# Optimization experiments

Hardware: AMD Instinct MI355X
Metric: run time of the kernel (lower is better)

Reference implementation:

```python
import jax, jax.numpy as jnp
import numpy as np

B, Q, D = 8, 900, 256
NH, DH = 8, 32
FF = 1024
NLEVELS, NPOINTS, NLAYERS = 4, 4, 6
SHAPES = [(100, 100), (50, 50), (25, 25), (13, 13)]
S = sum(h * w for h, w in SHAPES)  # 13294
EPS = 1e-5
SCALE = 1.0 / float(np.sqrt(DH))


def layer_norm(x, g, b):
    mu = jnp.mean(x, -1, keepdims=True)
    var = jnp.var(x, -1, keepdims=True)
    return (x - mu) * jax.lax.rsqrt(var + EPS) * g + b


def mha(x, wi, bi, wo, bo):
    qkv = x @ wi.T + bi
    q, k, v = jnp.split(qkv, 3, axis=-1)
    q = q.reshape(B, Q, NH, DH)
    k = k.reshape(B, Q, NH, DH)
    v = v.reshape(B, Q, NH, DH)
    attn = jax.nn.softmax(jnp.einsum('bqhd,bkhd->bhqk', q, k) * SCALE, -1)
    o = jnp.einsum('bhqk,bkhd->bqhd', attn, v).reshape(B, Q, D)
    return o @ wo.T + bo


def msda_core(value, loc, aw):
    # value (B,S,NH,DH); loc (B,Q,NH,L,P,2) in [0,1]; aw (B,Q,NH,L,P)
    v = value.transpose(0, 2, 1, 3)  # (B,NH,S,DH)
    out = jnp.zeros((B, NH, Q, DH), value.dtype)
    start = 0
    for lvl, (H_, W_) in enumerate(SHAPES):
        vl = v[:, :, start:start + H_ * W_]  # (B,NH,HW,DH)
        start += H_ * W_
        l = loc[:, :, :, lvl].transpose(0, 2, 1, 3, 4).reshape(B, NH, Q * NPOINTS, 2)
        # grid_sample align_corners=False pixel coords
        x = l[..., 0] * W_ - 0.5
        y = l[..., 1] * H_ - 0.5
        x0 = jnp.floor(x)
        y0 = jnp.floor(y)
        wx = x - x0
        wy = y - y0
        g = jnp.zeros((B, NH, Q * NPOINTS, DH), value.dtype)
        for dy, dx, w in ((0, 0, (1 - wx) * (1 - wy)), (0, 1, wx * (1 - wy)),
                          (1, 0, (1 - wx) * wy), (1, 1, wx * wy)):
            xi = x0 + dx
            yi = y0 + dy
            valid = ((xi >= 0) & (xi < W_) & (yi >= 0) & (yi < H_)).astype(value.dtype)
            idx = (jnp.clip(yi, 0, H_ - 1) * W_ + jnp.clip(xi, 0, W_ - 1)).astype(jnp.int32)
            gi = jnp.take_along_axis(vl, idx[..., None], axis=2)  # (B,NH,QP,DH)
            g = g + gi * (w * valid)[..., None]
        g = g.reshape(B, NH, Q, NPOINTS, DH)
        a = aw[:, :, :, lvl].transpose(0, 2, 1, 3)  # (B,NH,Q,P)
        out = out + jnp.einsum('bhqpd,bhqp->bhqd', g, a)
    return out.transpose(0, 2, 1, 3).reshape(B, Q, D)


def msda(query, ref, value_in, vp_w, vp_b, so_w, so_b, aw_w, aw_b, op_w, op_b):
    value = (value_in @ vp_w.T + vp_b).reshape(B, S, NH, DH)
    off = (query @ so_w.T + so_b).reshape(B, Q, NH, NLEVELS, NPOINTS, 2)
    aw = (query @ aw_w.T + aw_b).reshape(B, Q, NH, NLEVELS * NPOINTS)
    aw = jax.nn.softmax(aw, -1).reshape(B, Q, NH, NLEVELS, NPOINTS)
    # offset normalizer is (W, H) per level
    norm = jnp.array([[w, h] for h, w in SHAPES], jnp.float32)
    loc = ref[:, :, None, :, None, :] + off / norm[None, None, None, :, None, :]
    return msda_core(value, loc, aw) @ op_w.T + op_b


def setup_inputs():
    key = jax.random.key(0)
    it = iter(jax.random.split(key, 32))

    def rn(shape, s=0.02):
        return jax.random.normal(next(it), shape, jnp.float32) * s

    z = lambda n: jnp.zeros((n,), jnp.float32)
    o = lambda n: jnp.ones((n,), jnp.float32)
    NOFF = NH * NLEVELS * NPOINTS
    return {
        'tgt': rn((B, Q, D), 1.0),
        'reference_points': jax.random.uniform(next(it), (B, Q, 2), jnp.float32),
        'memory': rn((B, S, D), 1.0),
        'spatial_shapes': jnp.array(SHAPES, jnp.int32),
        'level_start_index': jnp.array(np.cumsum([0] + [h * w for h, w in SHAPES[:-1]]), jnp.int32),
        'valid_ratios': jnp.ones((B, NLEVELS, 2), jnp.float32),
        'query_pos': rn((B, Q, D), 1.0),
        'sa_in_w': rn((3 * D, D)), 'sa_in_b': z(3 * D),
        'sa_out_w': rn((D, D)), 'sa_out_b': z(D),
        'n1_g': o(D), 'n1_b': z(D),
        'n2_g': o(D), 'n2_b': z(D),
        'n3_g': o(D), 'n3_b': z(D),
        'vp_w': rn((D, D)), 'vp_b': z(D),
        'so_w': rn((NOFF * 2, D)), 'so_b': rn((NOFF * 2,), 0.5),
        'aw_w': rn((NOFF, D)), 'aw_b': z(NOFF),
        'op_w': rn((D, D)), 'op_b': z(D),
        'ff1_w': rn((FF, D)), 'ff1_b': z(FF),
        'ff2_w': rn((D, FF)), 'ff2_b': z(D),
    }


def reference(tgt, reference_points, memory, spatial_shapes, level_start_index,
              valid_ratios, query_pos,
              sa_in_w, sa_in_b, sa_out_w, sa_out_b,
              n1_g, n1_b, n2_g, n2_b, n3_g, n3_b,
              vp_w, vp_b, so_w, so_b, aw_w, aw_b, op_w, op_b,
              ff1_w, ff1_b, ff2_w, ff2_b):
    # NOTE: nn.ModuleList([decoder_layer]*num_layers) in the source shares one
    # layer's weights across all 6 layers; bbox_embed is None so reference
    # points are constant across layers.
    output = tgt
    ref_input = reference_points[:, :, None, :] * valid_ratios[:, None, :, :]  # (B,Q,L,2)
    inter, inter_refs = [], []
    for _ in range(NLAYERS):
        output = output + query_pos
        t2 = mha(output, sa_in_w, sa_in_b, sa_out_w, sa_out_b)
        output = layer_norm(output + t2, n1_g, n1_b)
        t2 = msda(output, ref_input, memory, vp_w, vp_b, so_w, so_b, aw_w, aw_b, op_w, op_b)
        output = layer_norm(output + t2, n2_g, n2_b)
        t2 = jax.nn.relu(output @ ff1_w.T + ff1_b) @ ff2_w.T + ff2_b
        output = layer_norm(output + t2, n3_g, n3_b)
        inter.append(output)
        inter_refs.append(reference_points)
    return (jnp.stack(inter), jnp.stack(inter_refs))
```

## Files before the change

### kernel.cpp

```cpp
#include <hip/hip_runtime.h>
#include <hip/hip_bf16.h>

typedef __hip_bfloat16 bf16;
typedef __bf16 bf16x8 __attribute__((ext_vector_type(8)));
typedef float  f32x4  __attribute__((ext_vector_type(4)));

#define NB 8
#define NQ 900
#define DM 256
#define NHEADS 8
#define DHEAD 32
#define NFF 1024
#define NLAY 6
#define NS 13294
#define BQ (NB*NQ)
#define LN_EPS 1e-5f
#define ATT_SCALE 0.17677669529663687f
#define SAK 40
#define VWS 264
#define PSK 88

__device__ __forceinline__ float bfd(const bf16* p, size_t i){ return __bfloat162float(p[i]); }

__device__ __forceinline__ float ldv(const void* p, size_t i, int mode, bool extF32)
{
    if (mode == 0) return ((const float*)p)[i];
    if (mode == 1) return bfd((const bf16*)p, i);
    return extF32 ? ((const float*)p)[i] : bfd((const bf16*)p, i);
}

__device__ __forceinline__ void unpack8(uint4 u, float* t)
{
    t[0] = __uint_as_float((u.x & 0xffffu) << 16);
    t[1] = __uint_as_float(u.x & 0xffff0000u);
    t[2] = __uint_as_float((u.y & 0xffffu) << 16);
    t[3] = __uint_as_float(u.y & 0xffff0000u);
    t[4] = __uint_as_float((u.z & 0xffffu) << 16);
    t[5] = __uint_as_float(u.z & 0xffff0000u);
    t[6] = __uint_as_float((u.w & 0xffffu) << 16);
    t[7] = __uint_as_float(u.w & 0xffff0000u);
}

__global__ __launch_bounds__(256) void detect_dtype(const void* __restrict__ tgt,
        float* __restrict__ flag)
{
    __shared__ float red[256];
    int t = threadIdx.x;
    const unsigned short* u = (const unsigned short*)tgt;
    float m = 0.f;
    for (int i = t; i < 2048; i += 256) {
        unsigned int bits = ((unsigned int)u[i]) << 16;
        float v = fabsf(__uint_as_float(bits));
        if (!isfinite(v)) v = 1e30f;
        m = fmaxf(m, v);
    }
    red[t] = m;
    __syncthreads();
    for (int st = 128; st; st >>= 1) {
        if (t < st) red[t] = fmaxf(red[t], red[t + st]);
        __syncthreads();
    }
    if (t == 0) flag[0] = (red[0] > 1e8f) ? 1.f : 0.f;
}

__global__ __launch_bounds__(256) void convert_w(const void* __restrict__ src,
        bf16* __restrict__ dst, const float* __restrict__ flagp)
{
    const bool ef = flagp[0] > 0.5f;
    size_t base = ((size_t)blockIdx.x * 256 + threadIdx.x) * 8;
    if (ef) {
        const float* s = (const float*)src + base;
        float4 f0 = *(const float4*)s;
        float4 f1 = *(const float4*)(s + 4);
        union { bf16 a[8]; uint4 u; } t;
        t.a[0] = __float2bfloat16(f0.x); t.a[1] = __float2bfloat16(f0.y);
        t.a[2] = __float2bfloat16(f0.z); t.a[3] = __float2bfloat16(f0.w);
        t.a[4] = __float2bfloat16(f1.x); t.a[5] = __float2bfloat16(f1.y);
        t.a[6] = __float2bfloat16(f1.z); t.a[7] = __float2bfloat16(f1.w);
        *(uint4*)(dst + base) = t.u;
    } else {
        *(uint4*)(dst + base) = *(const uint4*)((const bf16*)src + base);
    }
}

__global__ __launch_bounds__(256, 2) void gemm_vp(const void* __restrict__ A,
        const bf16* __restrict__ Wb, const void* __restrict__ bias,
        bf16* __restrict__ C, int M, const float* __restrict__ flagp)
{
    const bool ef = flagp[0] > 0.5f;
    __shared__ __align__(16) bf16 Al[64 * VWS];
    const int tid = threadIdx.x;
    const int w = tid >> 6, lane = tid & 63, lm = lane & 15, lq = lane >> 4;
    const int wq = w * 64;

    bf16x8 wf[4][8];
    #pragma unroll
    for (int nt = 0; nt < 4; nt++)
        #pragma unroll
        for (int ks = 0; ks < 8; ks++)
            wf[nt][ks] = *(const bf16x8*)(Wb +
                (size_t)(wq + nt * 16 + lm) * 256 + ks * 32 + lq * 8);

    float bv[4];
    #pragma unroll
    for (int nt = 0; nt < 4; nt++) bv[nt] = ldv(bias, wq + nt * 16 + lm, 2, ef);

    const int arow_l = tid >> 2;
    const int asub   = tid & 3;

    const int ntiles = (M + 63) / 64;
    for (int tile = blockIdx.x; tile < ntiles; tile += gridDim.x) {
        const int m0 = tile * 64;
        __syncthreads();
        {
            const int grow = m0 + arow_l;
            if (grow < M) {
                if (ef) {
                    const float* ap = (const float*)A + (size_t)grow * 256;
                    #pragma unroll
                    for (int j = 0; j < 16; j++) {
                        int colf = j * 16 + asub * 4;
                        float4 f = *(const float4*)(ap + colf);
                        union { bf16 a[4]; uint2 u; } t;
                        t.a[0] = __float2bfloat16(f.x); t.a[1] = __float2bfloat16(f.y);
                        t.a[2] = __float2bfloat16(f.z); t.a[3] = __float2bfloat16(f.w);
                        *(uint2*)&Al[arow_l * VWS + colf] = t.u;
                    }
                } else {
                    const bf16* ap = (const bf16*)A + (size_t)grow * 256;
                    #pragma unroll
                    for (int j = 0; j < 8; j++) {
                        int cole = j * 32 + asub * 8;
                        *(uint4*)&Al[arow_l * VWS + cole] = *(const uint4*)(ap + cole);
                    }
                }
            } else {
                uint4 z = make_uint4(0u, 0u, 0u, 0u);
                #pragma unroll
                for (int j = 0; j < 8; j++)
                    *(uint4*)&Al[arow_l * VWS + j * 32 + asub * 8] = z;
            }
        }
        __syncthreads();

        f32x4 acc[4][4];
        #pragma unroll
        for (int mi = 0; mi < 4; mi++)
            #pragma unroll
            for (int nt = 0; nt < 4; nt++)
                acc[mi][nt] = (f32x4){0.f, 0.f, 0.f, 0.f};

        #pragma unroll
        for (int ks = 0; ks < 8; ks++) {
            bf16x8 af[4];
            #pragma unroll
            for (int mi = 0; mi < 4; mi++)
                af[mi] = *(const bf16x8*)&Al[(mi * 16 + lm) * VWS + ks * 32 + lq * 8];
            #pragma unroll
            for (int nt = 0; nt < 4; nt++)
                #pragma unroll
                for (int mi = 0; mi < 4; mi++)
                    acc[mi][nt] = __builtin_amdgcn_mfma_f32_16x16x32_bf16(
                                      af[mi], wf[nt][ks], acc[mi][nt], 0, 0, 0);
        }

        #pragma unroll
        for (int mi = 0; mi < 4; mi++) {
            #pragma unroll
            for (int r = 0; r < 4; r++) {
                int m = m0 + mi * 16 + lq * 4 + r;
                if (m >= M) continue;
                #pragma unroll
                for (int nt = 0; nt < 4; nt++) {
                    int col = wq + nt * 16 + lm;
                    C[(size_t)m * 256 + col] = __float2bfloat16(acc[mi][nt][r] + bv[nt]);
                }
            }
        }
    }
}

__global__ __launch_bounds__(256, 2) void gemm_wreg(const bf16* __restrict__ A,
        const bf16* __restrict__ Wb, const void* __restrict__ bias,
        void* __restrict__ C, int cmode, int M, int N, int relu,
        const float* __restrict__ flagp)
{
    const bool ef = flagp[0] > 0.5f;
    __shared__ __align__(16) bf16 Al[32 * VWS];
    const int tid = threadIdx.x;
    const int w = tid >> 6, lane = tid & 63, lm = lane & 15, lq = lane >> 4;
    const int n0 = blockIdx.x * 256;
    const int m0 = blockIdx.y * 32;
    const int wq = n0 + w * 64;

    bf16x8 wf[4][8];
    #pragma unroll
    for (int nt = 0; nt < 4; nt++)
        #pragma unroll
        for (int ks = 0; ks < 8; ks++)
            wf[nt][ks] = *(const bf16x8*)(Wb +
                (size_t)(wq + nt * 16 + lm) * 256 + ks * 32 + lq * 8);

    float bv[4];
    #pragma unroll
    for (int nt = 0; nt < 4; nt++) bv[nt] = ldv(bias, wq + nt * 16 + lm, 2, ef);

    {
        const int ar = tid >> 3, ac = (tid & 7) * 32;
        if (m0 + ar < M) {
            const bf16* ap = A + (size_t)(m0 + ar) * 256 + ac;
            #pragma unroll
            for (int j = 0; j < 4; j++)
                *(uint4*)&Al[ar * VWS + ac + j * 8] = *(const uint4*)(ap + j * 8);
        } else {
            uint4 z = make_uint4(0u, 0u, 0u, 0u);
            #pragma unroll
            for (int j = 0; j < 4; j++)
                *(uint4*)&Al[ar * VWS + ac + j * 8] = z;
        }
    }
    __syncthreads();

    f32x4 acc[2][4];
    #pragma unroll
    for (int mi = 0; mi < 2; mi++)
        #pragma unroll
        for (int nt = 0; nt < 4; nt++)
            acc[mi][nt] = (f32x4){0.f, 0.f, 0.f, 0.f};

    #pragma unroll
    for (int ks = 0; ks < 8; ks++) {
        bf16x8 af[2];
        #pragma unroll
        for (int mi = 0; mi < 2; mi++)
            af[mi] = *(const bf16x8*)&Al[(mi * 16 + lm) * VWS + ks * 32 + lq * 8];
        #pragma unroll
        for (int nt = 0; nt < 4; nt++)
            #pragma unroll
            for (int mi = 0; mi < 2; mi++)
                acc[mi][nt] = __builtin_amdgcn_mfma_f32_16x16x32_bf16(
                                  af[mi], wf[nt][ks], acc[mi][nt], 0, 0, 0);
    }

    #pragma unroll
    for (int mi = 0; mi < 2; mi++) {
        #pragma unroll
        for (int r = 0; r < 4; r++) {
            int m = m0 + mi * 16 + lq * 4 + r;
            if (m >= M) continue;
            #pragma unroll
            for (int nt = 0; nt < 4; nt++) {
                int col = wq + nt * 16 + lm;
                float v = acc[mi][nt][r] + bv[nt];
                if (relu) v = fmaxf(v, 0.f);
                size_t ci = (size_t)m * N + col;
                if (cmode == 0) ((float*)C)[ci] = v;
                else            ((bf16*)C)[ci] = __float2bfloat16(v);
            }
        }
    }
}

__global__ __launch_bounds__(256, 2) void gemm_lnw(const bf16* __restrict__ A,
        const bf16* __restrict__ Wb, const void* __restrict__ bias,
        const float* __restrict__ res, const void* __restrict__ gw,
        const void* __restrict__ bw, float* __restrict__ out32,
        bf16* __restrict__ outbf, void* __restrict__ dout, size_t obase,
        const void* __restrict__ qp, int M,
        const float* __restrict__ flagp)
{
    const bool ef = flagp[0] > 0.5f;
    __shared__ __align__(16) bf16 Al[32 * VWS];
    const int tid = threadIdx.x;
    const int w = tid >> 6, lane = tid & 63, lm = lane & 15, lq = lane >> 4;
    const int m0 = blockIdx.y * 32;
    const int wq = w * 64;

    bf16x8 wf[4][8];
    #pragma unroll
    for (int nt = 0; nt < 4; nt++)
        #pragma unroll
        for (int ks = 0; ks < 8; ks++)
            wf[nt][ks] = *(const bf16x8*)(Wb +
                (size_t)(wq + nt * 16 + lm) * 256 + ks * 32 + lq * 8);

    float bias_c[4];
    #pragma unroll
    for (int nt = 0; nt < 4; nt++) bias_c[nt] = ldv(bias, wq + nt * 16 + lm, 2, ef);

    {
        const int ar = tid >> 3, ac = (tid & 7) * 32;
        if (m0 + ar < M) {
            const bf16* ap = A + (size_t)(m0 + ar) * 256 + ac;
            #pragma unroll
            for (int j = 0; j < 4; j++)
                *(uint4*)&Al[ar * VWS + ac + j * 8] = *(const uint4*)(ap + j * 8);
        } else {
            uint4 z = make_uint4(0u, 0u, 0u, 0u);
            #pragma unroll
            for (int j = 0; j < 4; j++)
                *(uint4*)&Al[ar * VWS + ac + j * 8] = z;
        }
    }
    __syncthreads();

    f32x4 acc[2][4];
    #pragma unroll
    for (int mi = 0; mi < 2; mi++)
        #pragma unroll
        for (int nt = 0; nt < 4; nt++)
            acc[mi][nt] = (f32x4){0.f, 0.f, 0.f, 0.f};

    #pragma unroll
    for (int ks = 0; ks < 8; ks++) {
        bf16x8 af[2];
        #pragma unroll
        for (int mi = 0; mi < 2; mi++)
            af[mi] = *(const bf16x8*)&Al[(mi * 16 + lm) * VWS + ks * 32 + lq * 8];
        #pragma unroll
        for (int nt = 0; nt < 4; nt++)
            #pragma unroll
            for (int mi = 0; mi < 2; mi++)
                acc[mi][nt] = __builtin_amdgcn_mfma_f32_16x16x32_bf16(
                                  af[mi], wf[nt][ks], acc[mi][nt], 0, 0, 0);
    }

    #pragma unroll
    for (int mi = 0; mi < 2; mi++)
        #pragma unroll
        for (int r = 0; r < 4; r++) {
            int row = m0 + mi * 16 + lq * 4 + r;
            bool vr_ = row < M;
            #pragma unroll
            for (int nt = 0; nt < 4; nt++) {
                int col = wq + nt * 16 + lm;
                float rv = vr_ ? res[(size_t)row * DM + col] : 0.f;
                acc[mi][nt][r] += bias_c[nt] + rv;
            }
        }

    __syncthreads();
    float* red = (float*)Al;
    float mu[2][4], rstd[2][4];
    #pragma unroll
    for (int mi = 0; mi < 2; mi++)
        #pragma unroll
        for (int r = 0; r < 4; r++) {
            float s = acc[mi][0][r] + acc[mi][1][r] + acc[mi][2][r] + acc[mi][3][r];
            s += __shfl_xor(s, 1, 64); s += __shfl_xor(s, 2, 64);
            s += __shfl_xor(s, 4, 64); s += __shfl_xor(s, 8, 64);
            if (lm == 0) red[(mi * 16 + lq * 4 + r) * 4 + w] = s;
        }
    __syncthreads();
    #pragma unroll
    for (int mi = 0; mi < 2; mi++)
        #pragma unroll
        for (int r = 0; r < 4; r++) {
            int ri = mi * 16 + lq * 4 + r;
            mu[mi][r] = (red[ri*4] + red[ri*4+1] + red[ri*4+2] + red[ri*4+3]) * (1.f / DM);
        }
    #pragma unroll
    for (int mi = 0; mi < 2; mi++)
        #pragma unroll
        for (int r = 0; r < 4; r++) {
            float q = 0.f;
            #pragma unroll
            for (int nt = 0; nt < 4; nt++) {
                float d = acc[mi][nt][r] - mu[mi][r];
                q += d * d;
            }
            q += __shfl_xor(q, 1, 64); q += __shfl_xor(q, 2, 64);
            q += __shfl_xor(q, 4, 64); q += __shfl_xor(q, 8, 64);
            if (lm == 0) red[128 + (mi * 16 + lq * 4 + r) * 4 + w] = q;
        }
    __syncthreads();
    #pragma unroll
    for (int mi = 0; mi < 2; mi++)
        #pragma unroll
        for (int r = 0; r < 4; r++) {
            int ri = mi * 16 + lq * 4 + r;
            float var = (red[128+ri*4] + red[128+ri*4+1] + red[128+ri*4+2] + red[128+ri*4+3]) * (1.f / DM);
            rstd[mi][r] = rsqrtf(var + LN_EPS);
        }

    float gcol[4], bcol[4];
    #pragma unroll
    for (int nt = 0; nt < 4; nt++) {
        int col = wq + nt * 16 + lm;
        gcol[nt] = ldv(gw, col, 2, ef);
        bcol[nt] = ldv(bw, col, 2, ef);
    }
    #pragma unroll
    for (int mi = 0; mi < 2; mi++)
        #pragma unroll
        for (int r = 0; r < 4; r++) {
            int row = m0 + mi * 16 + lq * 4 + r;
            if (row >= M) continue;
            size_t rbase = (size_t)row * DM;
            #pragma unroll
            for (int nt = 0; nt < 4; nt++) {
                int col = wq + nt * 16 + lm;
                float o = (acc[mi][nt][r] - mu[mi][r]) * rstd[mi][r] * gcol[nt] + bcol[nt];
                if (dout) {
                    if (ef) ((float*)dout)[obase + rbase + col] = o;
                    else    ((bf16*)dout)[obase + rbase + col] = __float2bfloat16(o);
                }
                float o2 = o + (qp ? ldv(qp, rbase + col, 2, ef) : 0.f);
                out32[rbase + col] = o2;
                outbf[rbase + col] = __float2bfloat16(o2);
            }
        }
}

__device__ __forceinline__ void stage_a32(bf16* As, const void* A, bool a_bf16,
        int m0, int M, int K, int k0, int tid)
{
    const int row = tid >> 3, col = (tid & 7) * 4;
    const int arow = m0 + row;
    union { bf16 a[4]; uint2 u; } t;
    if (arow < M) {
        size_t base = (size_t)arow * K + k0 + col;
        if (a_bf16) {
            t.u = *(const uint2*)((const bf16*)A + base);
        } else {
            float4 f = *(const float4*)((const float*)A + base);
            t.a[0] = __float2bfloat16(f.x); t.a[1] = __float2bfloat16(f.y);
            t.a[2] = __float2bfloat16(f.z); t.a[3] = __float2bfloat16(f.w);
        }
    } else {
        t.u = make_uint2(0u, 0u);
    }
    *(uint2*)&As[row * SAK + col] = t.u;
}

__global__ __launch_bounds__(256) void gemm_ln(const bf16* __restrict__ A,
        const bf16* __restrict__ Wb, const void* __restrict__ bias,
        const float* __restrict__ res, const void* __restrict__ gw,
        const void* __restrict__ bw, float* __restrict__ out32,
        bf16* __restrict__ outbf, void* __restrict__ dout, size_t obase,
        const void* __restrict__ qp, int M, int K,
        const float* __restrict__ flagp)
{
    const bool ef = flagp[0] > 0.5f;
    __shared__ __align__(16) bf16 As[32 * SAK];
    __shared__ __align__(16) bf16 Ws[256 * SAK];
    const int tid = threadIdx.x;
    const int m0 = blockIdx.y * 32;
    const int w = tid >> 6, lane = tid & 63, lm = lane & 15, lq = lane >> 4;
    const int wr = w >> 1, wc = w & 1;
    const int srow = tid >> 2, scol = (tid & 3) * 8;

    f32x4 acc[8];
    #pragma unroll
    for (int nt = 0; nt < 8; nt++) acc[nt] = (f32x4){0.f, 0.f, 0.f, 0.f};

    for (int k0 = 0; k0 < K; k0 += 32) {
        stage_a32(As, A, true, m0, M, K, k0, tid);
        #pragma unroll
        for (int it = 0; it < 4; it++) {
            int rr = it * 64 + srow;
            *(uint4*)&Ws[rr * SAK + scol] =
                *(const uint4*)(Wb + (size_t)rr * K + k0 + scol);
        }
        __syncthreads();

        bf16x8 af = *(const bf16x8*)&As[(wr * 16 + lm) * SAK + lq * 8];
        #pragma unroll
        for (int nt = 0; nt < 8; nt++) {
            bf16x8 bfr = *(const bf16x8*)&Ws[(wc * 128 + nt * 16 + lm) * SAK + lq * 8];
            acc[nt] = __builtin_amdgcn_mfma_f32_16x16x32_bf16(af, bfr, acc[nt], 0, 0, 0);
        }
        __syncthreads();
    }

    float bias_c[8], gcol[8], bcol[8];
    #pragma unroll
    for (int nt = 0; nt < 8; nt++) {
        int col = wc * 128 + nt * 16 + lm;
        bias_c[nt] = ldv(bias, col, 2, ef);
        gcol[nt]   = ldv(gw,   col, 2, ef);
        bcol[nt]   = ldv(bw,   col, 2, ef);
    }
    #pragma unroll
    for (int r = 0; r < 4; r++) {
        int row = m0 + wr * 16 + lq * 4 + r;
        bool vr_ = row < M;
        #pragma unroll
        for (int nt = 0; nt < 8; nt++) {
            int col = wc * 128 + nt * 16 + lm;
            float rv = vr_ ? res[(size_t)row * DM + col] : 0.f;
            acc[nt][r] += bias_c[nt] + rv;
        }
    }

    float* red = (float*)As;
    float mu[4], rstd[4];
    #pragma unroll
    for (int r = 0; r < 4; r++) {
        float s = 0.f;
        #pragma unroll
        for (int nt = 0; nt < 8; nt++) s += acc[nt][r];
        s += __shfl_xor(s, 1, 64); s += __shfl_xor(s, 2, 64);
        s += __shfl_xor(s, 4, 64); s += __shfl_xor(s, 8, 64);
        if (lm == 0) red[(wr * 16 + lq * 4 + r) * 2 + wc] = s;
    }
    __syncthreads();
    #pragma unroll
    for (int r = 0; r < 4; r++) {
        int rl = wr * 16 + lq * 4 + r;
        mu[r] = (red[rl * 2] + red[rl * 2 + 1]) * (1.f / DM);
    }
    #pragma unroll
    for (int r = 0; r < 4; r++) {
        float q = 0.f;
        #pragma unroll
        for (int nt = 0; nt < 8; nt++) {
            float d = acc[nt][r] - mu[r];
            q += d * d;
        }
        q += __shfl_xor(q, 1, 64); q += __shfl_xor(q, 2, 64);
        q += __shfl_xor(q, 4, 64); q += __shfl_xor(q, 8, 64);
        if (lm == 0) red[64 + (wr * 16 + lq * 4 + r) * 2 + wc] = q;
    }
    __syncthreads();
    #pragma unroll
    for (int r = 0; r < 4; r++) {
        int rl = wr * 16 + lq * 4 + r;
        float var = (red[64 + rl * 2] + red[64 + rl * 2 + 1]) * (1.f / DM);
        rstd[r] = rsqrtf(var + LN_EPS);
    }

    #pragma unroll
    for (int r = 0; r < 4; r++) {
        int row = m0 + wr * 16 + lq * 4 + r;
        if (row >= M) continue;
        size_t rbase = (size_t)row * DM;
        #pragma unroll
        for (int nt = 0; nt < 8; nt++) {
            int col = wc * 128 + nt * 16 + lm;
            float o = (acc[nt][r] - mu[r]) * rstd[r] * gcol[nt] + bcol[nt];
            if (dout) {
                if (ef) ((float*)dout)[obase + rbase + col] = o;
                else    ((bf16*)dout)[obase + rbase + col] = __float2bfloat16(o);
            }
            float o2 = o + (qp ? ldv(qp, rbase + col, 2, ef) : 0.f);
            out32[rbase + col] = o2;
            outbf[rbase + col] = __float2bfloat16(o2);
        }
    }
}

__global__ __launch_bounds__(256) void gemm_soaw(const bf16* __restrict__ A,
        const bf16* __restrict__ Wb, const void* __restrict__ b1,
        const void* __restrict__ b2, float* __restrict__ C1,
        float* __restrict__ C2, int M, const float* __restrict__ flagp)
{
    const bool ef = flagp[0] > 0.5f;
    const int K = DM;
    __shared__ __align__(16) bf16 As[32 * SAK];
    __shared__ __align__(16) bf16 Ws[128 * SAK];
    const int tid = threadIdx.x;
    const int m0 = blockIdx.y * 32, n0 = blockIdx.x * 128;
    const int w = tid >> 6, lane = tid & 63, lm = lane & 15, lq = lane >> 4;
    const int wr = w >> 1, wc = w & 1;
    const int srow = tid >> 2, scol = (tid & 3) * 8;

    f32x4 acc[4];
    #pragma unroll
    for (int nt = 0; nt < 4; nt++) acc[nt] = (f32x4){0.f, 0.f, 0.f, 0.f};

    for (int k0 = 0; k0 < K; k0 += 32) {
        stage_a32(As, A, true, m0, M, K, k0, tid);
        #pragma unroll
        for (int it = 0; it < 2; it++) {
            int rr = it * 64 + srow;
            *(uint4*)&Ws[rr * SAK + scol] =
                *(const uint4*)(Wb + (size_t)(n0 + rr) * K + k0 + scol);
        }
        __syncthreads();

        bf16x8 af = *(const bf16x8*)&As[(wr * 16 + lm) * SAK + lq * 8];
        #pragma unroll
        for (int nt = 0; nt < 4; nt++) {
            bf16x8 bfr = *(const bf16x8*)&Ws[(wc * 64 + nt * 16 + lm) * SAK + lq * 8];
            acc[nt] = __builtin_amdgcn_mfma_f32_16x16x32_bf16(af, bfr, acc[nt], 0, 0, 0);
        }
        __syncthreads();
    }

    float* Cd; const void* bsrc; int nst, c0;
    if (n0 < 256) { Cd = C1; bsrc = b1; nst = 256; c0 = n0; }
    else          { Cd = C2; bsrc = b2; nst = 128; c0 = n0 - 256; }

    #pragma unroll
    for (int nt = 0; nt < 4; nt++) {
        int cl = wc * 64 + nt * 16 + lm;
        float bv = ldv(bsrc, c0 + cl, 2, ef);
        #pragma unroll
        for (int r = 0; r < 4; r++) {
            int m = m0 + wr * 16 + lq * 4 + r;
            if (m >= M) continue;
            Cd[(size_t)m * nst + c0 + cl] = acc[nt][r] + bv;
        }
    }
}

__global__ __launch_bounds__(256) void add_qpos(const void* __restrict__ a, int amode,
        const void* __restrict__ qp, float* __restrict__ o, bf16* __restrict__ ob,
        const float* __restrict__ flagp)
{
    const bool ef = flagp[0] > 0.5f;
    int i = blockIdx.x * 256 + threadIdx.x;
    float v = ldv(a, i, amode, ef) + ldv(qp, i, 2, ef);
    o[i]  = v;
    ob[i] = __float2bfloat16(v);
}

__global__ __launch_bounds__(256) void mha_mfma(const bf16* __restrict__ qkv,
        bf16* __restrict__ out)
{
    const int qt = blockIdx.x, h = blockIdx.y, b = blockIdx.z;
    const int q0 = qt * 64;
    const int tid = threadIdx.x;
    const int w = tid >> 6, lane = tid & 63;
    const int lm = lane & 15, lq = lane >> 4;
    const int srow = tid >> 2, sc = (tid & 3) * 8;

    __shared__ __align__(16) bf16 Qs[64][SAK];
    __shared__ __align__(16) bf16 Ks[64][SAK];
    __shared__ __align__(16) bf16 Vt[32][66];
    __shared__ __align__(16) bf16 Ps[64][PSK];

    const bf16* base = qkv + (size_t)b * NQ * 768;

    {
        bf16 tmp[8];
        if (q0 + srow < NQ) {
            uint4 u = *(const uint4*)(base + (size_t)(q0 + srow) * 768 + h * DHEAD + sc);
            float t[8]; unpack8(u, t);
            #pragma unroll
            for (int i = 0; i < 8; i++) tmp[i] = __float2bfloat16(t[i] * ATT_SCALE);
        } else {
            #pragma unroll
            for (int i = 0; i < 8; i++) tmp[i] = __float2bfloat16(0.f);
        }
        *(uint4*)&Qs[srow][sc] = *(const uint4*)tmp;
    }
    __syncthreads();
    const bf16x8 qf = *(const bf16x8*)&Qs[w * 16 + lm][lq * 8];

    f32x4 O[2] = {{0.f,0.f,0.f,0.f},{0.f,0.f,0.f,0.f}};
    float mrow = -1e30f, lrow = 0.f;

    for (int k0 = 0; k0 < NQ; k0 += 64) {
        __syncthreads();
        {
            uint4 uk = {0u,0u,0u,0u}, uv = {0u,0u,0u,0u};
            if (k0 + srow < NQ) {
                const bf16* rp = base + (size_t)(k0 + srow) * 768 + h * DHEAD + sc;
                uk = *(const uint4*)(rp + 256);
                uv = *(const uint4*)(rp + 512);
            }
            *(uint4*)&Ks[srow][sc] = uk;
            const bf16* vv = (const bf16*)&uv;
            #pragma unroll
            for (int i = 0; i < 8; i++) Vt[sc + i][srow] = vv[i];
        }
        __syncthreads();

        float sv[16];
        #pragma unroll
        for (int mt = 0; mt < 4; mt++) {
            bf16x8 kf = *(const bf16x8*)&Ks[mt * 16 + lm][lq * 8];
            f32x4 d = __builtin_amdgcn_mfma_f32_16x16x32_bf16(kf, qf,
                        (f32x4){0.f,0.f,0.f,0.f}, 0, 0, 0);
            sv[mt*4+0] = d[0]; sv[mt*4+1] = d[1]; sv[mt*4+2] = d[2]; sv[mt*4+3] = d[3];
        }
        #pragma unroll
        for (int mt = 0; mt < 4; mt++)
            #pragma unroll
            for (int r = 0; r < 4; r++)
                if (k0 + mt * 16 + lq * 4 + r >= NQ) sv[mt*4+r] = -1e30f;

        float tmax = sv[0];
        #pragma unroll
        for (int j = 1; j < 16; j++) tmax = fmaxf(tmax, sv[j]);
        tmax = fmaxf(tmax, __shfl_xor(tmax, 16, 64));
        tmax = fmaxf(tmax, __shfl_xor(tmax, 32, 64));
        float mnew = fmaxf(mrow, tmax);
        float alpha = __expf(mrow - mnew);
        mrow = mnew;
        float psum = 0.f;
        #pragma unroll
        for (int j = 0; j < 16; j++) {
            float p = __expf(sv[j] - mnew);
            sv[j] = p; psum += p;
        }
        psum += __shfl_xor(psum, 16, 64);
        psum += __shfl_xor(psum, 32, 64);
        lrow = lrow * alpha + psum;

        #pragma unroll
        for (int mt = 0; mt < 4; mt++) {
            union { bf16 a[4]; uint2 u; } pw;
            #pragma unroll
            for (int r = 0; r < 4; r++) pw.a[r] = __float2bfloat16(sv[mt*4+r]);
            *(uint2*)&Ps[w * 16 + lm][mt * 16 + lq * 4] = pw.u;
        }

        #pragma unroll
        for (int mt = 0; mt < 2; mt++)
            #pragma unroll
            for (int r = 0; r < 4; r++) O[mt][r] *= alpha;
        #pragma unroll
        for (int ks = 0; ks < 2; ks++) {
            bf16x8 pf = *(const bf16x8*)&Ps[w * 16 + lm][ks * 32 + lq * 8];
            #pragma unroll
            for (int mt = 0; mt < 2; mt++) {
                bf16x8 vf = *(const bf16x8*)&Vt[mt * 16 + lm][ks * 32 + lq * 8];
                O[mt] = __builtin_amdgcn_mfma_f32_16x16x32_bf16(vf, pf, O[mt], 0, 0, 0);
            }
        }
    }

    int q = q0 + w * 16 + lm;
    if (q < NQ) {
        float invl = 1.f / lrow;
        bf16* op = out + ((size_t)(b * NQ + q)) * DM + h * DHEAD;
        #pragma unroll
        for (int mt = 0; mt < 2; mt++)
            #pragma unroll
            for (int r = 0; r < 4; r++)
                op[mt * 16 + lq * 4 + r] = __float2bfloat16(O[mt][r] * invl);
    }
}

__global__ __launch_bounds__(256) void msda_sample8(const bf16* __restrict__ value,
        const float* __restrict__ off, const float* __restrict__ aw,
        const void* __restrict__ refp, const void* __restrict__ vr,
        bf16* __restrict__ out, const float* __restrict__ flagp)
{
    const bool ef = flagp[0] > 0.5f;
    const int tid = threadIdx.x;
    const int bq0 = blockIdx.x * 8;

    __shared__ float sOff[8][256];
    __shared__ float sAw[8][128];
    __shared__ float sref[8][2];
    __shared__ float svrq[8][8];

    {
        const float* osrc = off + (size_t)bq0 * 256;
        #pragma unroll
        for (int i = 0; i < 2; i++) {
            int e = i * 1024 + tid * 4;
            *(float4*)&sOff[e >> 8][e & 255] = *(const float4*)(osrc + e);
        }
        int e2 = tid * 4;
        *(float4*)&sAw[e2 >> 7][e2 & 127] = *(const float4*)(aw + (size_t)bq0 * 128 + e2);
    }
    if (tid < 16) sref[tid >> 1][tid & 1] = ldv(refp, (size_t)(bq0 + (tid >> 1)) * 2 + (tid & 1), 2, ef);
    if (tid < 64) {
        int qi = tid >> 3, j = tid & 7;
        int b = (bq0 + qi) / NQ;
        svrq[qi][j] = ldv(vr, b * 8 + j, 2, ef);
    }
    __syncthreads();

    if (tid < 64) {
        int qi = tid >> 3, h = tid & 7;
        float* p = &sAw[qi][h * 16];
        float mx = -1e30f;
        #pragma unroll
        for (int j = 0; j < 16; j++) mx = fmaxf(mx, p[j]);
        float s = 0.f;
        #pragma unroll
        for (int j = 0; j < 16; j++) { float e = __expf(p[j] - mx); p[j] = e; s += e; }
        float inv = 1.f / s;
        #pragma unroll
        for (int j = 0; j < 16; j++) p[j] *= inv;
    }
    __syncthreads();

    const int qi = tid >> 5, sub = tid & 31;
    const int h = sub >> 2, cg = sub & 3;
    const int bq = bq0 + qi;
    const int b = bq / NQ;
    const bf16* vb = value + (size_t)b * NS * DM + h * DHEAD + cg * 8;

    float acc[8];
    #pragma unroll
    for (int j = 0; j < 8; j++) acc[j] = 0.f;

    const int HS[4] = {100, 50, 25, 13};
    const int ST[4] = {0, 10000, 12500, 13125};
    #pragma unroll
    for (int lvl = 0; lvl < 4; lvl++) {
        const int W_ = HS[lvl], H_ = HS[lvl], st = ST[lvl];
        float rx = sref[qi][0] * svrq[qi][lvl * 2 + 0] * (float)W_;
        float ry = sref[qi][1] * svrq[qi][lvl * 2 + 1] * (float)H_;
        #pragma unroll
        for (int p = 0; p < 4; p++) {
            int oi = h * 32 + lvl * 8 + p * 2;
            float x = fminf(fmaxf(rx + sOff[qi][oi]     - 0.5f, -4.f), (float)W_ + 4.f);
            float y = fminf(fmaxf(ry + sOff[qi][oi + 1] - 0.5f, -4.f), (float)H_ + 4.f);
            float x0f = floorf(x), y0f = floorf(y);
            float wx = x - x0f, wy = y - y0f;
            int x0 = (int)x0f, y0 = (int)y0f;
            int x1i = x0 + 1, y1i = y0 + 1;
            bool vx0 = (x0 >= 0) && (x0 < W_), vx1 = (x1i >= 0) && (x1i < W_);
            bool vy0 = (y0 >= 0) && (y0 < H_), vy1 = (y1i >= 0) && (y1i < H_);
            float g[8];
            #pragma unroll
            for (int j = 0; j < 8; j++) g[j] = 0.f;
            float t[8];
            if (vy0) {
                int rowo = (st + y0 * W_) * DM;
                if (vx0) {
                    uint4 u = *(const uint4*)(vb + rowo + x0 * DM);
                    unpack8(u, t);
                    float wgt = (1.f - wx) * (1.f - wy);
                    #pragma unroll
                    for (int j = 0; j < 8; j++) g[j] += wgt * t[j];
                }
                if (vx1) {
                    uint4 u = *(const uint4*)(vb + rowo + x1i * DM);
                    unpack8(u, t);
                    float wgt = wx * (1.f - wy);
                    #pragma unroll
                    for (int j = 0; j < 8; j++) g[j] += wgt * t[j];
                }
            }
            if (vy1) {
                int rowo = (st + y1i * W_) * DM;
                if (vx0) {
                    uint4 u = *(const uint4*)(vb + rowo + x0 * DM);
                    unpack8(u, t);
                    float wgt = (1.f - wx) * wy;
                    #pragma unroll
                    for (int j = 0; j < 8; j++) g[j] += wgt * t[j];
                }
                if (vx1) {
                    uint4 u = *(const uint4*)(vb + rowo + x1i * DM);
                    unpack8(u, t);
                    float wgt = wx * wy;
                    #pragma unroll
                    for (int j = 0; j < 8; j++) g[j] += wgt * t[j];
                }
            }
            float a = sAw[qi][h * 16 + lvl * 4 + p];
            #pragma unroll
            for (int j = 0; j < 8; j++) acc[j] += a * g[j];
        }
    }

    union { bf16 t[8]; uint4 u; } pk;
    #pragma unroll
    for (int j = 0; j < 8; j++) pk.t[j] = __float2bfloat16(acc[j]);
    *(uint4*)(out + (size_t)bq * DM + h * DHEAD + cg * 8) = pk.u;
}

__global__ __launch_bounds__(256) void copy_refs(const void* __restrict__ refp,
        void* __restrict__ out, const float* __restrict__ flagp)
{
    const bool ef = flagp[0] > 0.5f;
    int i = blockIdx.x * 256 + threadIdx.x;
    if (i >= NLAY * BQ * 2) return;
    float v = ldv(refp, i % (BQ * 2), 2, ef);
    size_t oi = (size_t)NLAY * BQ * DM + i;
    if (ef) ((float*)out)[oi] = v;
    else    ((bf16*)out)[oi] = __float2bfloat16(v);
}

extern "C" void kernel_launch(void* const* d_in, const int* in_sizes, int n_in,
                              void* d_out, int out_size, void* d_ws, size_t ws_size,
                              hipStream_t stream)
{
    const void* tgt     = d_in[0];
    const void* refp    = d_in[1];
    const void* memory  = d_in[2];
    const void* vr      = d_in[5];
    const void* qp      = d_in[6];
    const void* sa_in_w = d_in[7];
    const void* sa_in_b = d_in[8];
    const void* sa_out_w= d_in[9];
    const void* sa_out_b= d_in[10];
    const void* n1_g    = d_in[11];
    const void* n1_b    = d_in[12];
    const void* n2_g    = d_in[13];
    const void* n2_b    = d_in[14];
    const void* n3_g    = d_in[15];
    const void* n3_b    = d_in[16];
    const void* vp_w    = d_in[17];
    const void* vp_b    = d_in[18];
    const void* so_w    = d_in[19];
    const void* so_b    = d_in[20];
    const void* aw_w    = d_in[21];
    const void* aw_b    = d_in[22];
    const void* op_w    = d_in[23];
    const void* op_b    = d_in[24];
    const void* ff1_w   = d_in[25];
    const void* ff1_b   = d_in[26];
    const void* ff2_w   = d_in[27];
    const void* ff2_b   = d_in[28];

    char* w = (char*)d_ws;
    float* flagp  = (float*)w;  w += 256;
    bf16*  value  = (bf16*)w;   w += (size_t)NB * NS * DM * 2;
    float* outbuf = (float*)w;  w += (size_t)BQ * DM * 4;
    float* x1samp = (float*)w;  w += (size_t)BQ * DM * 4;
    bf16*  bigb   = (bf16*)w;   w += (size_t)BQ * NFF * 2;
    float* attoff = (float*)w;  w += (size_t)BQ * DM * 4;
    float* awb    = (float*)w;  w += (size_t)BQ * 128 * 4;
    bf16*  abuf   = (bf16*)w;   w += (size_t)BQ * DM * 2;
    bf16*  outbf  = (bf16*)w;   w += (size_t)BQ * DM * 2;
    bf16* wb_sa_in = (bf16*)w;  w += (size_t)768 * 256 * 2;
    bf16* wb_sa_out= (bf16*)w;  w += (size_t)256 * 256 * 2;
    bf16* wb_soaw  = (bf16*)w;  w += (size_t)384 * 256 * 2;
    bf16* wb_op    = (bf16*)w;  w += (size_t)256 * 256 * 2;
    bf16* wb_ff1   = (bf16*)w;  w += (size_t)NFF * 256 * 2;
    bf16* wb_ff2   = (bf16*)w;  w += (size_t)256 * NFF * 2;
    bf16* wb_vp    = (bf16*)w;  w += (size_t)256 * 256 * 2;

    const int gy = (BQ + 31) / 32;
    const int MV = NB * NS;

    detect_dtype<<<1, 256, 0, stream>>>(tgt, flagp);
    convert_w<<< 96, 256, 0, stream>>>(sa_in_w,  wb_sa_in,  flagp);
    convert_w<<< 32, 256, 0, stream>>>(sa_out_w, wb_sa_out, flagp);
    convert_w<<< 32, 256, 0, stream>>>(so_w,     wb_soaw,   flagp);
    convert_w<<< 16, 256, 0, stream>>>(aw_w,     wb_soaw + 256 * 256, flagp);
    convert_w<<< 32, 256, 0, stream>>>(op_w,     wb_op,     flagp);
    convert_w<<<128, 256, 0, stream>>>(ff1_w,    wb_ff1,    flagp);
    convert_w<<<128, 256, 0, stream>>>(ff2_w,    wb_ff2,    flagp);
    convert_w<<< 32, 256, 0, stream>>>(vp_w,     wb_vp,     flagp);

    gemm_vp<<<512, 256, 0, stream>>>(memory, wb_vp, vp_b, value, MV, flagp);

    copy_refs<<<(NLAY * BQ * 2 + 255) / 256, 256, 0, stream>>>(refp, d_out, flagp);

    add_qpos<<<BQ * DM / 256, 256, 0, stream>>>(tgt, 2, qp, x1samp, abuf, flagp);

    for (int l = 0; l < NLAY; l++) {
        gemm_wreg<<<dim3(3, gy), 256, 0, stream>>>(
            abuf, wb_sa_in, sa_in_b, bigb, 1, BQ, 768, 0, flagp);
        mha_mfma<<<dim3(15, NHEADS, NB), 256, 0, stream>>>(bigb, abuf);
        gemm_lnw<<<dim3(1, gy), 256, 0, stream>>>(
            abuf, wb_sa_out, sa_out_b, x1samp, n1_g, n1_b,
            outbuf, outbf, nullptr, 0, nullptr, BQ, flagp);

        gemm_soaw<<<dim3(3, gy), 256, 0, stream>>>(
            outbf, wb_soaw, so_b, aw_b, attoff, awb, BQ, flagp);
        msda_sample8<<<BQ / 8, 256, 0, stream>>>(value, attoff, awb, refp, vr, abuf, flagp);
        gemm_lnw<<<dim3(1, gy), 256, 0, stream>>>(
            abuf, wb_op, op_b, outbuf, n2_g, n2_b,
            outbuf, outbf, nullptr, 0, nullptr, BQ, flagp);

        gemm_wreg<<<dim3(4, gy), 256, 0, stream>>>(
            outbf, wb_ff1, ff1_b, bigb, 1, BQ, 1024, 1, flagp);
        gemm_ln<<<dim3(1, gy), 256, 0, stream>>>(
            bigb, wb_ff2, ff2_b, outbuf, n3_g, n3_b,
            x1samp, abuf, d_out, (size_t)l * BQ * DM, qp, BQ, NFF, flagp);
    }
}
```

Baseline: 1.486 ms.

## Halve row tile of LN-fused GEMMs and restage FF2 with resident A rows

The fused GEMM+LayerNorm kernel for the attention and deformable-attention output projections now processes 16 rows per block instead of 32. This doubles the grid (450 vs 225 blocks) so more CUs are busy, and it uses a small dedicated reduction buffer. The FF2+LN kernel is replaced by gemm_ffln, which keeps a full 16x1024 A tile in shared memory and streams the 256-wide weight in 64-K chunks, with each wave owning 64 output columns. The trade-off is that each block re-reads the whole weight matrix for half as many rows, doubling total weight traffic, and the kernel uses a large LDS footprint (~69KB), which may limit occupancy.

Result: slower. 1.523 ms (+2.5%).

```diff
diff --git a/kernel.cpp b/kernel.cpp
--- a/kernel.cpp
+++ b/kernel.cpp
@@ -19,6 +19,8 @@
 #define SAK 40
 #define VWS 264
 #define PSK 88
+#define AFS 1032
+#define WS2 72
 
 __device__ __forceinline__ float bfd(const bf16* p, size_t i){ return __bfloat162float(p[i]); }
 
@@ -270,10 +272,11 @@
         const float* __restrict__ flagp)
 {
     const bool ef = flagp[0] > 0.5f;
-    __shared__ __align__(16) bf16 Al[32 * VWS];
+    __shared__ __align__(16) bf16 Al[16 * VWS];
+    __shared__ float red[128];
     const int tid = threadIdx.x;
     const int w = tid >> 6, lane = tid & 63, lm = lane & 15, lq = lane >> 4;
-    const int m0 = blockIdx.y * 32;
+    const int m0 = blockIdx.y * 16;
     const int wq = w * 64;
 
     bf16x8 wf[4][8];
@@ -289,99 +292,77 @@
     for (int nt = 0; nt < 4; nt++) bias_c[nt] = ldv(bias, wq + nt * 16 + lm, 2, ef);
 
     {
-        const int ar = tid >> 3, ac = (tid & 7) * 32;
+        const int ar = tid >> 4, ac = (tid & 15) * 16;
         if (m0 + ar < M) {
             const bf16* ap = A + (size_t)(m0 + ar) * 256 + ac;
-            #pragma unroll
-            for (int j = 0; j < 4; j++)
-                *(uint4*)&Al[ar * VWS + ac + j * 8] = *(const uint4*)(ap + j * 8);
+            *(uint4*)&Al[ar * VWS + ac]     = *(const uint4*)ap;
+            *(uint4*)&Al[ar * VWS + ac + 8] = *(const uint4*)(ap + 8);
         } else {
             uint4 z = make_uint4(0u, 0u, 0u, 0u);
-            #pragma unroll
-            for (int j = 0; j < 4; j++)
-                *(uint4*)&Al[ar * VWS + ac + j * 8] = z;
-        }
-    }
-    __syncthreads();
-
-    f32x4 acc[2][4];
-    #pragma unroll
-    for (int mi = 0; mi < 2; mi++)
+            *(uint4*)&Al[ar * VWS + ac]     = z;
+            *(uint4*)&Al[ar * VWS + ac + 8] = z;
+        }
+    }
+    __syncthreads();
+
+    f32x4 acc[4];
+    #pragma unroll
+    for (int nt = 0; nt < 4; nt++) acc[nt] = (f32x4){0.f, 0.f, 0.f, 0.f};
+
+    #pragma unroll
+    for (int ks = 0; ks < 8; ks++) {
+        bf16x8 af = *(const bf16x8*)&Al[lm * VWS + ks * 32 + lq * 8];
         #pragma unroll
         for (int nt = 0; nt < 4; nt++)
-            acc[mi][nt] = (f32x4){0.f, 0.f, 0.f, 0.f};
-
-    #pragma unroll
-    for (int ks = 0; ks < 8; ks++) {
-        bf16x8 af[2];
-        #pragma unroll
-        for (int mi = 0; mi < 2; mi++)
-            af[mi] = *(const bf16x8*)&Al[(mi * 16 + lm) * VWS + ks * 32 + lq * 8];
-        #pragma unroll
-        for (int nt = 0; nt < 4; nt++)
-            #pragma unroll
-            for (int mi = 0; mi < 2; mi++)
-                acc[mi][nt] = __builtin_amdgcn_mfma_f32_16x16x32_bf16(
-                                  af[mi], wf[nt][ks], acc[mi][nt], 0, 0, 0);
-    }
-
-    #pragma unroll
-    for (int mi = 0; mi < 2; mi++)
-        #pragma unroll
-        for (int r = 0; r < 4; r++) {
-            int row = m0 + mi * 16 + lq * 4 + r;
-            bool vr_ = row < M;
-            #pragma unroll
-            for (int nt = 0; nt < 4; nt++) {
-                int col = wq + nt * 16 + lm;
-                float rv = vr_ ? res[(size_t)row * DM + col] : 0.f;
-                acc[mi][nt][r] += bias_c[nt] + rv;
-            }
-        }
-
-    __syncthreads();
-    float* red = (float*)Al;
-    float mu[2][4], rstd[2][4];
-    #pragma unroll
-    for (int mi = 0; mi < 2; mi++)
-        #pragma unroll
-        for (int r = 0; r < 4; r++) {
-            float s = acc[mi][0][r] + acc[mi][1][r] + acc[mi][2][r] + acc[mi][3][r];
-            s += __shfl_xor(s, 1, 64); s += __shfl_xor(s, 2, 64);
-            s += __shfl_xor(s, 4, 64); s += __shfl_xor(s, 8, 64);
-            if (lm == 0) red[(mi * 16 + lq * 4 + r) * 4 + w] = s;
-        }
-    __syncthreads();
-    #pragma unroll
-    for (int mi = 0; mi < 2; mi++)
-        #pragma unroll
-        for (int r = 0; r < 4; r++) {
-            int ri = mi * 16 + lq * 4 + r;
-            mu[mi][r] = (red[ri*4] + red[ri*4+1] + red[ri*4+2] + red[ri*4+3]) * (1.f / DM);
-        }
-    #pragma unroll
-    for (int mi = 0; mi < 2; mi++)
-        #pragma unroll
-        for (int r = 0; r < 4; r++) {
-            float q = 0.f;
-            #pragma unroll
-            for (int nt = 0; nt < 4; nt++) {
-                float d = acc[mi][nt][r] - mu[mi][r];
-                q += d * d;
-            }
-            q += __shfl_xor(q, 1, 64); q += __shfl_xor(q, 2, 64);
-            q += __shfl_xor(q, 4, 64); q += __shfl_xor(q, 8, 64);
-            if (lm == 0) red[128 + (mi * 16 + lq * 4 + r) * 4 + w] = q;
-        }
-    __syncthreads();
-    #pragma unroll
-    for (int mi = 0; mi < 2; mi++)
-        #pragma unroll
-        for (int r = 0; r < 4; r++) {
-            int ri = mi * 16 + lq * 4 + r;
-            float var = (red[128+ri*4] + red[128+ri*4+1] + red[128+ri*4+2] + red[128+ri*4+3]) * (1.f / DM);
-            rstd[mi][r] = rsqrtf(var + LN_EPS);
-        }
+            acc[nt] = __builtin_amdgcn_mfma_f32_16x16x32_bf16(
+                          af, wf[nt][ks], acc[nt], 0, 0, 0);
+    }
+
+    #pragma unroll
+    for (int r = 0; r < 4; r++) {
+        int row = m0 + lq * 4 + r;
+        bool vr_ = row < M;
+        #pragma unroll
+        for (int nt = 0; nt < 4; nt++) {
+            int col = wq + nt * 16 + lm;
+            float rv = vr_ ? res[(size_t)row * DM + col] : 0.f;
+            acc[nt][r] += bias_c[nt] + rv;
+        }
+    }
+
+    float mu[4], rstd[4];
+    #pragma unroll
+    for (int r = 0; r < 4; r++) {
+        float s = acc[0][r] + acc[1][r] + acc[2][r] + acc[3][r];
+        s += __shfl_xor(s, 1, 64); s += __shfl_xor(s, 2, 64);
+        s += __shfl_xor(s, 4, 64); s += __shfl_xor(s, 8, 64);
+        if (lm == 0) red[(lq * 4 + r) * 4 + w] = s;
+    }
+    __syncthreads();
+    #pragma unroll
+    for (int r = 0; r < 4; r++) {
+        int ri = lq * 4 + r;
+        mu[r] = (red[ri*4] + red[ri*4+1] + red[ri*4+2] + red[ri*4+3]) * (1.f / DM);
+    }
+    #pragma unroll
+    for (int r = 0; r < 4; r++) {
+        float q = 0.f;
+        #pragma unroll
+        for (int nt = 0; nt < 4; nt++) {
+            float d = acc[nt][r] - mu[r];
+            q += d * d;
+        }
+        q += __shfl_xor(q, 1, 64); q += __shfl_xor(q, 2, 64);
+        q += __shfl_xor(q, 4, 64); q += __shfl_xor(q, 8, 64);
+        if (lm == 0) red[64 + (lq * 4 + r) * 4 + w] = q;
+    }
+    __syncthreads();
+    #pragma unroll
+    for (int r = 0; r < 4; r++) {
+        int ri = lq * 4 + r;
+        float var = (red[64+ri*4] + red[64+ri*4+1] + red[64+ri*4+2] + red[64+ri*4+3]) * (1.f / DM);
+        rstd[r] = rsqrtf(var + LN_EPS);
+    }
 
     float gcol[4], bcol[4];
     #pragma unroll
@@ -391,25 +372,158 @@
         bcol[nt] = ldv(bw, col, 2, ef);
     }
     #pragma unroll
-    for (int mi = 0; mi < 2; mi++)
-        #pragma unroll
-        for (int r = 0; r < 4; r++) {
-            int row = m0 + mi * 16 + lq * 4 + r;
-            if (row >= M) continue;
-            size_t rbase = (size_t)row * DM;
+    for (int r = 0; r < 4; r++) {
+        int row = m0 + lq * 4 + r;
+        if (row >= M) continue;
+        size_t rbase = (size_t)row * DM;
+        #pragma unroll
+        for (int nt = 0; nt < 4; nt++) {
+            int col = wq + nt * 16 + lm;
+            float o = (acc[nt][r] - mu[r]) * rstd[r] * gcol[nt] + bcol[nt];
+            if (dout) {
+                if (ef) ((float*)dout)[obase + rbase + col] = o;
+                else    ((bf16*)dout)[obase + rbase + col] = __float2bfloat16(o);
+            }
+            float o2 = o + (qp ? ldv(qp, rbase + col, 2, ef) : 0.f);
+            out32[rbase + col] = o2;
+            outbf[rbase + col] = __float2bfloat16(o2);
+        }
+    }
+}
+
+__global__ __launch_bounds__(256, 2) void gemm_ffln(const bf16* __restrict__ A,
+        const bf16* __restrict__ Wb, const void* __restrict__ bias,
+        const float* __restrict__ res, const void* __restrict__ gw,
+        const void* __restrict__ bw, float* __restrict__ out32,
+        bf16* __restrict__ outbf, void* __restrict__ dout, size_t obase,
+        const void* __restrict__ qp, int M,
+        const float* __restrict__ flagp)
+{
+    const bool ef = flagp[0] > 0.5f;
+    __shared__ __align__(16) bf16 Aff[16 * AFS];
+    __shared__ __align__(16) bf16 Ws2[256 * WS2];
+    __shared__ float red[128];
+    const int tid = threadIdx.x;
+    const int w = tid >> 6, lane = tid & 63, lm = lane & 15, lq = lane >> 4;
+    const int m0 = blockIdx.y * 16;
+    const int wq = w * 64;
+
+    {
+        const int ar = tid >> 4, ac = (tid & 15) * 64;
+        if (m0 + ar < M) {
+            const bf16* ap = A + (size_t)(m0 + ar) * NFF + ac;
+            #pragma unroll
+            for (int j = 0; j < 8; j++)
+                *(uint4*)&Aff[ar * AFS + ac + j * 8] = *(const uint4*)(ap + j * 8);
+        } else {
+            uint4 z = make_uint4(0u, 0u, 0u, 0u);
+            #pragma unroll
+            for (int j = 0; j < 8; j++)
+                *(uint4*)&Aff[ar * AFS + ac + j * 8] = z;
+        }
+    }
+
+    f32x4 acc[4];
+    #pragma unroll
+    for (int nt = 0; nt < 4; nt++) acc[nt] = (f32x4){0.f, 0.f, 0.f, 0.f};
+
+    for (int k0 = 0; k0 < NFF; k0 += 64) {
+        __syncthreads();
+        {
+            const bf16* wp = Wb + (size_t)tid * NFF + k0;
+            #pragma unroll
+            for (int j = 0; j < 8; j++)
+                *(uint4*)&Ws2[tid * WS2 + j * 8] = *(const uint4*)(wp + j * 8);
+        }
+        __syncthreads();
+
+        #pragma unroll
+        for (int ks = 0; ks < 2; ks++) {
+            bf16x8 af = *(const bf16x8*)&Aff[lm * AFS + k0 + ks * 32 + lq * 8];
             #pragma unroll
             for (int nt = 0; nt < 4; nt++) {
-                int col = wq + nt * 16 + lm;
-                float o = (acc[mi][nt][r] - mu[mi][r]) * rstd[mi][r] * gcol[nt] + bcol[nt];
-                if (dout) {
-                    if (ef) ((float*)dout)[obase + rbase + col] = o;
-                    else    ((bf16*)dout)[obase + rbase + col] = __float2bfloat16(o);
-                }
-                float o2 = o + (qp ? ldv(qp, rbase + col, 2, ef) : 0.f);
-                out32[rbase + col] = o2;
-                outbf[rbase + col] = __float2bfloat16(o2);
+                bf16x8 bfr = *(const bf16x8*)&Ws2[(wq + nt * 16 + lm) * WS2 + ks * 32 + lq * 8];
+                acc[nt] = __builtin_amdgcn_mfma_f32_16x16x32_bf16(
+                              af, bfr, acc[nt], 0, 0, 0);
             }
         }
+    }
+
+    float bias_c[4];
+    #pragma unroll
+    for (int nt = 0; nt < 4; nt++) bias_c[nt] = ldv(bias, wq + nt * 16 + lm, 2, ef);
+    #pragma unroll
+    for (int r = 0; r < 4; r++) {
+        int row = m0 + lq * 4 + r;
+        bool vr_ = row < M;
+        #pragma unroll
+        for (int nt = 0; nt < 4; nt++) {
+            int col = wq + nt * 16 + lm;
+            float rv = vr_ ? res[(size_t)row * DM + col] : 0.f;
+            acc[nt][r] += bias_c[nt] + rv;
+        }
+    }
+
+    __syncthreads();
+    float mu[4], rstd[4];
+    #pragma unroll
+    for (int r = 0; r < 4; r++) {
+        float s = acc[0][r] + acc[1][r] + acc[2][r] + acc[3][r];
+        s += __shfl_xor(s, 1, 64); s += __shfl_xor(s, 2, 64);
+        s += __shfl_xor(s, 4, 64); s += __shfl_xor(s, 8, 64);
+        if (lm == 0) red[(lq * 4 + r) * 4 + w] = s;
+    }
+    __syncthreads();
+    #pragma unroll
+    for (int r = 0; r < 4; r++) {
+        int ri = lq * 4 + r;
+        mu[r] = (red[ri*4] + red[ri*4+1] + red[ri*4+2] + red[ri*4+3]) * (1.f / DM);
+    }
+    #pragma unroll
+    for (int r = 0; r < 4; r++) {
+        float q = 0.f;
+        #pragma unroll
+        for (int nt = 0; nt < 4; nt++) {
+            float d = acc[nt][r] - mu[r];
+            q += d * d;
+        }
+        q += __shfl_xor(q, 1, 64); q += __shfl_xor(q, 2, 64);
+        q += __shfl_xor(q, 4, 64); q += __shfl_xor(q, 8, 64);
+        if (lm == 0) red[64 + (lq * 4 + r) * 4 + w] = q;
+    }
+    __syncthreads();
+    #pragma unroll
+    for (int r = 0; r < 4; r++) {
+        int ri = lq * 4 + r;
+        float var = (red[64+ri*4] + red[64+ri*4+1] + red[64+ri*4+2] + red[64+ri*4+3]) * (1.f / DM);
+        rstd[r] = rsqrtf(var + LN_EPS);
+    }
+
+    float gcol[4], bcol[4];
+    #pragma unroll
+    for (int nt = 0; nt < 4; nt++) {
+        int col = wq + nt * 16 + lm;
+        gcol[nt] = ldv(gw, col, 2, ef);
+        bcol[nt] = ldv(bw, col, 2, ef);
+    }
+    #pragma unroll
+    for (int r = 0; r < 4; r++) {
+        int row = m0 + lq * 4 + r;
+        if (row >= M) continue;
+        size_t rbase = (size_t)row * DM;
+        #pragma unroll
+        for (int nt = 0; nt < 4; nt++) {
+            int col = wq + nt * 16 + lm;
+            float o = (acc[nt][r] - mu[r]) * rstd[r] * gcol[nt] + bcol[nt];
+            if (dout) {
+                if (ef) ((float*)dout)[obase + rbase + col] = o;
+                else    ((bf16*)dout)[obase + rbase + col] = __float2bfloat16(o);
+            }
+            float o2 = o + (qp ? ldv(qp, rbase + col, 2, ef) : 0.f);
+            out32[rbase + col] = o2;
+            outbf[rbase + col] = __float2bfloat16(o2);
+        }
+    }
 }
 
 __device__ __forceinline__ void stage_a32(bf16* As, const void* A, bool a_bf16,
@@ -431,123 +545,6 @@
         t.u = make_uint2(0u, 0u);
     }
     *(uint2*)&As[row * SAK + col] = t.u;
-}
-
-__global__ __launch_bounds__(256) void gemm_ln(const bf16* __restrict__ A,
-        const bf16* __restrict__ Wb, const void* __restrict__ bias,
-        const float* __restrict__ res, const void* __restrict__ gw,
-        const void* __restrict__ bw, float* __restrict__ out32,
-        bf16* __restrict__ outbf, void* __restrict__ dout, size_t obase,
-        const void* __restrict__ qp, int M, int K,
-        const float* __restrict__ flagp)
-{
-    const bool ef = flagp[0] > 0.5f;
-    __shared__ __align__(16) bf16 As[32 * SAK];
-    __shared__ __align__(16) bf16 Ws[256 * SAK];
-    const int tid = threadIdx.x;
-    const int m0 = blockIdx.y * 32;
-    const int w = tid >> 6, lane = tid & 63, lm = lane & 15, lq = lane >> 4;
-    const int wr = w >> 1, wc = w & 1;
-    const int srow = tid >> 2, scol = (tid & 3) * 8;
-
-    f32x4 acc[8];
-    #pragma unroll
-    for (int nt = 0; nt < 8; nt++) acc[nt] = (f32x4){0.f, 0.f, 0.f, 0.f};
-
-    for (int k0 = 0; k0 < K; k0 += 32) {
-        stage_a32(As, A, true, m0, M, K, k0, tid);
-        #pragma unroll
-        for (int it = 0; it < 4; it++) {
-            int rr = it * 64 + srow;
-            *(uint4*)&Ws[rr * SAK + scol] =
-                *(const uint4*)(Wb + (size_t)rr * K + k0 + scol);
-        }
-        __syncthreads();
-
-        bf16x8 af = *(const bf16x8*)&As[(wr * 16 + lm) * SAK + lq * 8];
-        #pragma unroll
-        for (int nt = 0; nt < 8; nt++) {
-            bf16x8 bfr = *(const bf16x8*)&Ws[(wc * 128 + nt * 16 + lm) * SAK + lq * 8];
-            acc[nt] = __builtin_amdgcn_mfma_f32_16x16x32_bf16(af, bfr, acc[nt], 0, 0, 0);
-        }
-        __syncthreads();
-    }
-
-    float bias_c[8], gcol[8], bcol[8];
-    #pragma unroll
-    for (int nt = 0; nt < 8; nt++) {
-        int col = wc * 128 + nt * 16 + lm;
-        bias_c[nt] = ldv(bias, col, 2, ef);
-        gcol[nt]   = ldv(gw,   col, 2, ef);
-        bcol[nt]   = ldv(bw,   col, 2, ef);
-    }
-    #pragma unroll
-    for (int r = 0; r < 4; r++) {
-        int row = m0 + wr * 16 + lq * 4 + r;
-        bool vr_ = row < M;
-        #pragma unroll
-        for (int nt = 0; nt < 8; nt++) {
-            int col = wc * 128 + nt * 16 + lm;
-            float rv = vr_ ? res[(size_t)row * DM + col] : 0.f;
-            acc[nt][r] += bias_c[nt] + rv;
-        }
-    }
-
-    float* red = (float*)As;
-    float mu[4], rstd[4];
-    #pragma unroll
-    for (int r = 0; r < 4; r++) {
-        float s = 0.f;
-        #pragma unroll
-        for (int nt = 0; nt < 8; nt++) s += acc[nt][r];
-        s += __shfl_xor(s, 1, 64); s += __shfl_xor(s, 2, 64);
-        s += __shfl_xor(s, 4, 64); s += __shfl_xor(s, 8, 64);
-        if (lm == 0) red[(wr * 16 + lq * 4 + r) * 2 + wc] = s;
-    }
-    __syncthreads();
-    #pragma unroll
-    for (int r = 0; r < 4; r++) {
-        int rl = wr * 16 + lq * 4 + r;
-        mu[r] = (red[rl * 2] + red[rl * 2 + 1]) * (1.f / DM);
-    }
-    #pragma unroll
-    for (int r = 0; r < 4; r++) {
-        float q = 0.f;
-        #pragma unroll
-        for (int nt = 0; nt < 8; nt++) {
-            float d = acc[nt][r] - mu[r];
-            q += d * d;
-        }
-        q += __shfl_xor(q, 1, 64); q += __shfl_xor(q, 2, 64);
-        q += __shfl_xor(q, 4, 64); q += __shfl_xor(q, 8, 64);
-        if (lm == 0) red[64 + (wr * 16 + lq * 4 + r) * 2 + wc] = q;
-    }
-    __syncthreads();
-    #pragma unroll
-    for (int r = 0; r < 4; r++) {
-        int rl = wr * 16 + lq * 4 + r;
-        float var = (red[64 + rl * 2] + red[64 + rl * 2 + 1]) * (1.f / DM);
-        rstd[r] = rsqrtf(var + LN_EPS);
-    }
-
-    #pragma unroll
-    for (int r = 0; r < 4; r++) {
-        int row = m0 + wr * 16 + lq * 4 + r;
-        if (row >= M) continue;
-        size_t rbase = (size_t)row * DM;
-        #pragma unroll
-        for (int nt = 0; nt < 8; nt++) {
-            int col = wc * 128 + nt * 16 + lm;
-            float o = (acc[nt][r] - mu[r]) * rstd[r] * gcol[nt] + bcol[nt];
-            if (dout) {
-                if (ef) ((float*)dout)[obase + rbase + col] = o;
-                else    ((bf16*)dout)[obase + rbase + col] = __float2bfloat16(o);
-            }
-            float o2 = o + (qp ? ldv(qp, rbase + col, 2, ef) : 0.f);
-            out32[rbase + col] = o2;
-            outbf[rbase + col] = __float2bfloat16(o2);
-        }
-    }
 }
 
 __global__ __launch_bounds__(256) void gemm_soaw(const bf16* __restrict__ A,
@@ -922,7 +919,8 @@
     bf16* wb_ff2   = (bf16*)w;  w += (size_t)256 * NFF * 2;
     bf16* wb_vp    = (bf16*)w;  w += (size_t)256 * 256 * 2;
 
-    const int gy = (BQ + 31) / 32;
+    const int gy  = (BQ + 31) / 32;
+    const int gy16 = (BQ + 15) / 16;
     const int MV = NB * NS;
 
     detect_dtype<<<1, 256, 0, stream>>>(tgt, flagp);
@@ -945,21 +943,21 @@
         gemm_wreg<<<dim3(3, gy), 256, 0, stream>>>(
             abuf, wb_sa_in, sa_in_b, bigb, 1, BQ, 768, 0, flagp);
         mha_mfma<<<dim3(15, NHEADS, NB), 256, 0, stream>>>(bigb, abuf);
-        gemm_lnw<<<dim3(1, gy), 256, 0, stream>>>(
+        gemm_lnw<<<dim3(1, gy16), 256, 0, stream>>>(
             abuf, wb_sa_out, sa_out_b, x1samp, n1_g, n1_b,
             outbuf, outbf, nullptr, 0, nullptr, BQ, flagp);
 
         gemm_soaw<<<dim3(3, gy), 256, 0, stream>>>(
             outbf, wb_soaw, so_b, aw_b, attoff, awb, BQ, flagp);
         msda_sample8<<<BQ / 8, 256, 0, stream>>>(value, attoff, awb, refp, vr, abuf, flagp);
-        gemm_lnw<<<dim3(1, gy), 256, 0, stream>>>(
+        gemm_lnw<<<dim3(1, gy16), 256, 0, stream>>>(
             abuf, wb_op, op_b, outbuf, n2_g, n2_b,
             outbuf, outbf, nullptr, 0, nullptr, BQ, flagp);
 
         gemm_wreg<<<dim3(4, gy), 256, 0, stream>>>(
             outbf, wb_ff1, ff1_b, bigb, 1, BQ, 1024, 1, flagp);
-        gemm_ln<<<dim3(1, gy), 256, 0, stream>>>(
+        gemm_ffln<<<dim3(1, gy16), 256, 0, stream>>>(
             bigb, wb_ff2, ff2_b, outbuf, n3_g, n3_b,
-            x1samp, abuf, d_out, (size_t)l * BQ * DM, qp, BQ, NFF, flagp);
-    }
-}
+            x1samp, abuf, d_out, (size_t)l * BQ * DM, qp, BQ, flagp);
+    }
+}
```
